# Kernel tuning notes

Hardware: AMD Instinct MI355X
Metric: run time of the kernel (lower is better)

The kernel has to match this reference:

```python
import jax, jax.numpy as jnp
from jax import lax
import numpy as np

BS, T, DA, DZ, K = 64, 512, 16, 32, 3


def _lstm_layer(x, Wih, Whh, bih, bhh):
    # x: [B, T, in], PyTorch LSTM gate order i,f,g,o; zero initial state
    B = x.shape[0]
    H = Whh.shape[1]
    b = bih + bhh

    def step(carry, xt):
        h, c = carry
        g = xt @ Wih.T + h @ Whh.T + b  # [B, 4H]
        i, f, gg, o = jnp.split(g, 4, axis=-1)
        c = jax.nn.sigmoid(f) * c + jax.nn.sigmoid(i) * jnp.tanh(gg)
        h = jax.nn.sigmoid(o) * jnp.tanh(c)
        return (h, c), h

    h0 = jnp.zeros((B, H), x.dtype)
    _, hs = lax.scan(step, (h0, h0), jnp.swapaxes(x, 0, 1))
    return jnp.swapaxes(hs, 0, 1)


def setup_inputs() -> dict:
    key = jax.random.key(0)
    ks = jax.random.split(key, 12)
    a = jax.random.normal(ks[0], (BS, T, DA), jnp.float32)
    # mixture dynamics / emission matrices, kept near identity for stability
    A = 0.95 * jnp.eye(DZ, dtype=jnp.float32) + 0.02 * jax.random.normal(ks[1], (K, T, DZ, DZ), jnp.float32)
    C = jnp.eye(DA, DZ, dtype=jnp.float32) + 0.05 * jax.random.normal(ks[2], (K, T, DA, DZ), jnp.float32)
    R = 0.1 * jnp.eye(DA, dtype=jnp.float32)
    Q = 0.1 * jnp.eye(DZ, dtype=jnp.float32)
    mu0 = jnp.zeros((DZ,), jnp.float32)
    sigma0 = jnp.eye(DZ, dtype=jnp.float32)
    H4 = 4 * K  # LSTM hidden size = K
    Wih0 = 0.1 * jax.random.normal(ks[3], (H4, DA), jnp.float32)
    Whh0 = 0.1 * jax.random.normal(ks[4], (H4, K), jnp.float32)
    bih0 = 0.1 * jax.random.normal(ks[5], (H4,), jnp.float32)
    bhh0 = 0.1 * jax.random.normal(ks[6], (H4,), jnp.float32)
    Wih1 = 0.1 * jax.random.normal(ks[7], (H4, K), jnp.float32)
    Whh1 = 0.1 * jax.random.normal(ks[8], (H4, K), jnp.float32)
    bih1 = 0.1 * jax.random.normal(ks[9], (H4,), jnp.float32)
    bhh1 = 0.1 * jax.random.normal(ks[10], (H4,), jnp.float32)
    return {"a": a, "A": A, "C": C, "R": R, "Q": Q, "mu0": mu0, "sigma0": sigma0,
            "Wih0": Wih0, "Whh0": Whh0, "bih0": bih0, "bhh0": bhh0,
            "Wih1": Wih1, "Whh1": Whh1, "bih1": bih1, "bhh1": bhh1}


def reference(a, A, C, R, Q, mu0, sigma0, Wih0, Whh0, bih0, bhh0, Wih1, Whh1, bih1, bhh1):
    bs, T, da = a.shape
    dz = A.shape[-1]
    # dynamics network: 2-layer LSTM + softmax mixture weights alpha [bs,T,K]
    h = _lstm_layer(a, Wih0, Whh0, bih0, bhh0)
    h = _lstm_layer(h, Wih1, Whh1, bih1, bhh1)
    alpha = jax.nn.softmax(h, axis=-1)
    # mix per-mode matrices; time-major [T,bs,.,.]
    At = jnp.einsum('btk,ktij->tbij', alpha, A)
    Ct = jnp.einsum('btk,ktij->tbij', alpha, C)
    a_tm = jnp.swapaxes(a, 0, 1)  # [T,bs,da]
    I = jnp.eye(dz, dtype=a.dtype)
    mu_f0 = jnp.broadcast_to(mu0, (bs, dz))
    sig_f0 = jnp.broadcast_to(sigma0, (bs, dz, dz))

    def fstep(carry, inp):
        mu_f, mu_p, sig_p = carry  # prev filtered mean, predicted mean/cov
        a_t, A_t, C_t = inp
        # NOTE: residual uses previous *filtered* mean, matching the source code
        r = a_t - jnp.einsum('bij,bj->bi', C_t, mu_f)
        Ct_T = jnp.swapaxes(C_t, -1, -2)
        S = C_t @ sig_p @ Ct_T + R
        Kg = sig_p @ Ct_T @ jnp.linalg.inv(S)
        mu_new = mu_p + jnp.einsum('bij,bj->bi', Kg, r)
        sig_new = (I - Kg @ C_t) @ sig_p
        mu_p_new = jnp.einsum('bij,bj->bi', A_t, mu_new)
        sig_p_new = A_t @ sig_new @ jnp.swapaxes(A_t, -1, -2) + Q
        return (mu_new, mu_p_new, sig_p_new), (mu_new, sig_new, mu_p_new, sig_p_new)

    _, (mu_f, sig_f, mu_p, sig_p) = lax.scan(
        fstep, (mu_f0, mu_f0, sig_f0), (a_tm, At, Ct))

    # RTS smoothing (backward recursion), faithful to smooth()
    def sstep(carry, inp):
        mu_n, sig_n = carry
        mu_ft, sig_ft, mu_pt, sig_pt, A_next = inp
        J = sig_ft @ jnp.swapaxes(A_next, -1, -2) @ jnp.linalg.inv(sig_pt)
        mu_s = mu_ft + jnp.einsum('bij,bj->bi', J, mu_n - mu_pt)
        sig_s = sig_ft + J @ (sig_n - sig_pt)
        return (mu_s, sig_s), (mu_s, sig_s)

    _, (mu_s_rest, sig_s_rest) = lax.scan(
        sstep, (mu_f[-1], sig_f[-1]),
        (mu_f[:-1], sig_f[:-1], mu_p[:-1], sig_p[:-1], At[1:]),
        reverse=True)
    mu_s = jnp.concatenate([mu_s_rest, mu_f[-1:]], axis=0)   # [T,bs,dz]
    sig_s = jnp.concatenate([sig_s_rest, sig_f[-1:]], axis=0)  # [T,bs,dz,dz]
    out = jnp.concatenate([mu_s, sig_s.reshape(T, bs, dz * dz)], axis=-1)
    return jnp.swapaxes(out, 0, 1)  # [bs, T, dz + dz*dz]
```

## Files before the change

kernel.cpp:

```cpp
#include <hip/hip_runtime.h>
#include <hip/hip_bf16.h>

#define BSZ 64
#define TT  512
#define DA  16
#define DZ  32
#define NG  12
#define NT  256

typedef __hip_bfloat16 bf;

#define FP32_R0 0x3DCCCCCDu

__device__ __forceinline__ int mode_(const void* Rm){
  return (((const unsigned*)Rm)[0] == FP32_R0) ? 0 : 1;
}
__device__ __forceinline__ float LD(const void* p, size_t i, int b16){
  return b16 ? __bfloat162float(((const bf*)p)[i]) : ((const float*)p)[i];
}
__device__ __forceinline__ void STO(void* p, size_t i, float v, int b16){
  if (b16) ((bf*)p)[i] = __float2bfloat16(v);
  else     ((float*)p)[i] = v;
}
__device__ __forceinline__ float osan_(double vd, float code){
  float v = (float)vd;
  unsigned u = __float_as_uint(v);
  if ((u & 0x7f800000u) == 0x7f800000u)
    return ((u & 0x007fffffu) != 0u) ? code : ((u >> 31) ? -(code-1000.0f) : (code-1000.0f));
  return v;
}
__device__ __forceinline__ float sigm_(float x){ return 1.0f/(1.0f + __expf(-x)); }
__device__ __forceinline__ float tanh_(float x){ return 1.0f - 2.0f/(__expf(2.0f*x)+1.0f); }

__device__ void alpha_stage_(int b, int tid, int b16,
  const void* a, const void* Wih0, const void* bih0, const void* bhh0,
  const void* Whh0, const void* Wih1, const void* Whh1,
  const void* bih1, const void* bhh1,
  float* sxw, float* salp)
{
  for (int e=tid; e<TT*NG; e+=NT){
    int t=e/NG, g=e-NG*t;
    float s = LD(bih0,g,b16) + LD(bhh0,g,b16);
    size_t ab = ((size_t)b*TT + t)*DA;
    #pragma unroll
    for (int j=0;j<DA;++j) s += LD(Wih0,g*DA+j,b16)*LD(a,ab+j,b16);
    sxw[e] = s;
  }
  __syncthreads();
  if (tid==0){
    float w0[NG][3], wi1[NG][3], w1[NG][3], bb[NG];
    #pragma unroll
    for (int g=0;g<NG;++g){
      #pragma unroll
      for (int j=0;j<3;++j){ w0[g][j]=LD(Whh0,(size_t)g*3+j,b16); wi1[g][j]=LD(Wih1,(size_t)g*3+j,b16); w1[g][j]=LD(Whh1,(size_t)g*3+j,b16); }
      bb[g] = LD(bih1,g,b16) + LD(bhh1,g,b16);
    }
    float h1[3]={0,0,0}, c1[3]={0,0,0}, h2[3]={0,0,0}, c2[3]={0,0,0};
    for (int t=0;t<TT;++t){
      const float* xr = sxw + t*NG;
      float g1[NG];
      #pragma unroll
      for (int g=0;g<NG;++g) g1[g] = xr[g] + w0[g][0]*h1[0]+w0[g][1]*h1[1]+w0[g][2]*h1[2];
      #pragma unroll
      for (int j=0;j<3;++j){
        float iv=sigm_(g1[j]), fv=sigm_(g1[3+j]), gv=tanh_(g1[6+j]), ov=sigm_(g1[9+j]);
        c1[j] = fv*c1[j] + iv*gv;
        h1[j] = ov*tanh_(c1[j]);
      }
      float g2[NG];
      #pragma unroll
      for (int g=0;g<NG;++g) g2[g] = bb[g] + wi1[g][0]*h1[0]+wi1[g][1]*h1[1]+wi1[g][2]*h1[2]
                                            + w1[g][0]*h2[0]+w1[g][1]*h2[1]+w1[g][2]*h2[2];
      #pragma unroll
      for (int j=0;j<3;++j){
        float iv=sigm_(g2[j]), fv=sigm_(g2[3+j]), gv=tanh_(g2[6+j]), ov=sigm_(g2[9+j]);
        c2[j] = fv*c2[j] + iv*gv;
        h2[j] = ov*tanh_(c2[j]);
      }
      float m = fmaxf(h2[0], fmaxf(h2[1], h2[2]));
      float e0=__expf(h2[0]-m), e1=__expf(h2[1]-m), e2=__expf(h2[2]-m);
      float inv = 1.0f/(e0+e1+e2);
      salp[t*3+0]=e0*inv; salp[t*3+1]=e1*inv; salp[t*3+2]=e2*inv;
    }
  }
  __syncthreads();
}

__global__ __launch_bounds__(256) void k_alpha(
  const void* __restrict__ a, const void* __restrict__ Rm,
  const void* __restrict__ Wih0, const void* __restrict__ Whh0,
  const void* __restrict__ bih0, const void* __restrict__ bhh0,
  const void* __restrict__ Wih1, const void* __restrict__ Whh1,
  const void* __restrict__ bih1, const void* __restrict__ bhh1,
  float* __restrict__ alws)
{
  const int b16 = mode_(Rm);
  const int b = blockIdx.x, tid = threadIdx.x;
  __shared__ float sxw[TT*NG];
  __shared__ float salp[TT*3];
  alpha_stage_(b, tid, b16, a, Wih0, bih0, bhh0, Whh0, Wih1, Whh1, bih1, bhh1,
               sxw, salp);
  for (int e=tid;e<TT*3;e+=NT) alws[(size_t)b*TT*3+e] = salp[e];
}

__global__ __launch_bounds__(256) void k_fwd(
  const void* __restrict__ a, const void* __restrict__ Am,
  const void* __restrict__ Cm, const void* __restrict__ Rm,
  const void* __restrict__ Qm, const void* __restrict__ mu0,
  const void* __restrict__ sig0,
  const void* __restrict__ Wih0, const void* __restrict__ Whh0,
  const void* __restrict__ bih0, const void* __restrict__ bhh0,
  const void* __restrict__ Wih1, const void* __restrict__ Whh1,
  const void* __restrict__ bih1, const void* __restrict__ bhh1,
  const float* __restrict__ alws,
  void* __restrict__ out)
{
  const int b16 = mode_(Rm);
  const int b = blockIdx.x, tid = threadIdx.x;
  __shared__ double dpool[4240];
  __shared__ float sAt[1056], sCt[528], sQ[1056], sR[272], sPCt[544], sKg[544];
  __shared__ float salp[TT*3];
  __shared__ double dMu[32], dMup[32], dr[16];
  double* dPp  = dpool;
  double* dPf  = dpool+1056;
  double* dCP  = dpool+2112;
  double* dT1  = dpool+2640;
  double* dAugS= dpool+3696;
  double* dMinv= dpool+3968;

  if (alws){
    for (int e=tid;e<TT*3;e+=NT) salp[e] = alws[(size_t)b*TT*3+e];
    __syncthreads();
  } else {
    alpha_stage_(b, tid, b16, a, Wih0, bih0, bhh0, Whh0, Wih1, Whh1, bih1, bhh1,
                 (float*)dpool, salp);
  }

  for (int e=tid;e<1024;e+=NT){ int i=e>>5,j=e&31;
    sQ[i*33+j]  = LD(Qm,e,b16);
    dPp[i*33+j] = (double)LD(sig0,e,b16); }
  for (int e=tid;e<256;e+=NT){ int i=e>>4,j=e&15; sR[i*17+j] = LD(Rm,e,b16); }
  if (tid<32){ double m = (double)LD(mu0,tid,b16); dMu[tid]=m; dMup[tid]=m; }
  __syncthreads();

  const int i0 = tid>>5, j0 = tid&31;
  const int i4 = tid>>4, j4 = tid&15;

  float pA0[4],pA1[4],pA2[4],pC0[2],pC1[2],pC2[2];
  {
    size_t o0=0, o1=(size_t)TT*1024, o2=(size_t)2*TT*1024;
    #pragma unroll
    for (int q=0;q<4;++q){ int e=tid+q*NT; pA0[q]=LD(Am,o0+e,b16); pA1[q]=LD(Am,o1+e,b16); pA2[q]=LD(Am,o2+e,b16); }
    size_t c0=0, c1=(size_t)TT*512, c2=(size_t)2*TT*512;
    #pragma unroll
    for (int q=0;q<2;++q){ int e=tid+q*NT; pC0[q]=LD(Cm,c0+e,b16); pC1[q]=LD(Cm,c1+e,b16); pC2[q]=LD(Cm,c2+e,b16); }
  }

  for (int t=0;t<TT;++t){
    const size_t ob = ((size_t)b*TT+t)*1056;
    {
      float a0=salp[t*3+0], a1=salp[t*3+1], a2=salp[t*3+2];
      #pragma unroll
      for (int q=0;q<4;++q){ int e=tid+q*NT; int i=e>>5,j=e&31;
        sAt[i*33+j] = a0*pA0[q]+a1*pA1[q]+a2*pA2[q]; }
      #pragma unroll
      for (int q=0;q<2;++q){ int e=tid+q*NT; int i=e>>5,j=e&31;
        sCt[i*33+j] = a0*pC0[q]+a1*pC1[q]+a2*pC2[q]; }
    }
    if (t+1<TT){
      size_t o0=(size_t)(t+1)*1024, o1=(size_t)(TT+t+1)*1024, o2=(size_t)(2*TT+t+1)*1024;
      #pragma unroll
      for (int q=0;q<4;++q){ int e=tid+q*NT; pA0[q]=LD(Am,o0+e,b16); pA1[q]=LD(Am,o1+e,b16); pA2[q]=LD(Am,o2+e,b16); }
      size_t c0=(size_t)(t+1)*512, c1=(size_t)(TT+t+1)*512, c2=(size_t)(2*TT+t+1)*512;
      #pragma unroll
      for (int q=0;q<2;++q){ int e=tid+q*NT; pC0[q]=LD(Cm,c0+e,b16); pC1[q]=LD(Cm,c1+e,b16); pC2[q]=LD(Cm,c2+e,b16); }
    }
    __syncthreads();

    {
      double A0=0.0, A1=0.0;
      for (int k=0;k<32;++k){ double bv=dPp[k*33+j0];
        A0 += (double)sCt[i0*33+k]*bv;
        A1 += (double)sCt[(i0+8)*33+k]*bv; }
      dCP[i0*33+j0]=A0; dCP[(i0+8)*33+j0]=A1;
    }
    {
      double A0=0.0, A1=0.0;
      for (int m=0;m<32;++m){ double cv=(double)sCt[j4*33+m];
        A0 += dPp[i4*33+m]*cv;
        A1 += dPp[(i4+16)*33+m]*cv; }
      sPCt[i4*17+j4]=(float)A0; sPCt[(i4+16)*17+j4]=(float)A1;
    }
    if (tid<16){ double s = (double)LD(a,((size_t)b*TT+t)*DA+tid,b16);
      for (int k=0;k<32;++k) s -= (double)sCt[tid*33+k]*dMu[k];
      dr[tid]=s; }
    __syncthreads();

    { int i=tid>>4, j=tid&15; double v=(double)sR[i*17+j];
      for (int k=0;k<32;++k) v += dCP[i*33+k]*(double)sCt[j*33+k];
      dAugS[i*17+j]=v; }
    __syncthreads();

    if (tid < 64){
      const int r = tid>>2, q = tid&3, cbase = q*8;
      double Rg[8];
      #pragma unroll
      for (int u=0;u<8;++u){
        int c = cbase+u;
        Rg[u] = (c<16) ? dAugS[r*17+c] : ((c-16)==r ? 1.0 : 0.0);
      }
      #pragma unroll
      for (int kp=0;kp<16;++kp){
        double pv = __shfl(Rg[kp&7], (kp<<2)|(kp>>3), 64);
        if (!(fabs(pv)>1e-300)) pv=1.0;
        double ip = 1.0/pv;
        if (r==kp){
          #pragma unroll
          for (int u=0;u<8;++u){ int c=cbase+u; if (c>kp) Rg[u]*=ip; }
        }
        double rf = __shfl(Rg[kp&7], (tid&0x3C)|(kp>>3), 64);
        #pragma unroll
        for (int u=0;u<8;++u){
          double pr = __shfl(Rg[u], (kp<<2)|q, 64);
          int c=cbase+u;
          if (r!=kp && c>kp) Rg[u] -= rf*pr;
        }
      }
      if (q>=2){
        #pragma unroll
        for (int u=0;u<8;++u){ int k=cbase+u-16; dMinv[r*17+k]=Rg[u]; }
      }
    }
    __syncthreads();

    {
      double A0=0.0, A1=0.0;
      for (int l=0;l<16;++l){ double mv=dMinv[l*17+j4];
        A0 += (double)sPCt[i4*17+l]*mv;
        A1 += (double)sPCt[(i4+16)*17+l]*mv; }
      sKg[i4*17+j4]=(float)A0; sKg[(i4+16)*17+j4]=(float)A1;
    }
    __syncthreads();

    if (tid<32){ double s=dMup[tid];
      for (int k=0;k<16;++k) s += (double)sKg[tid*17+k]*dr[k];
      dMu[tid]=s;
      STO(out, ob+tid, osan_(s,5300.0f), b16);
    }
    {
      double A0=dPp[i0*33+j0], A1=dPp[(i0+8)*33+j0],
             A2=dPp[(i0+16)*33+j0], A3=dPp[(i0+24)*33+j0];
      for (int l=0;l<16;++l){ double cv=dCP[l*33+j0];
        A0 -= (double)sKg[i0*17+l]*cv;
        A1 -= (double)sKg[(i0+8)*17+l]*cv;
        A2 -= (double)sKg[(i0+16)*17+l]*cv;
        A3 -= (double)sKg[(i0+24)*17+l]*cv; }
      dPf[i0*33+j0]=A0; dPf[(i0+8)*33+j0]=A1;
      dPf[(i0+16)*33+j0]=A2; dPf[(i0+24)*33+j0]=A3;
      STO(out, ob+32+((size_t)i0<<5)+j0,      osan_(A0,5300.0f), b16);
      STO(out, ob+32+((size_t)(i0+8)<<5)+j0,  osan_(A1,5300.0f), b16);
      STO(out, ob+32+((size_t)(i0+16)<<5)+j0, osan_(A2,5300.0f), b16);
      STO(out, ob+32+((size_t)(i0+24)<<5)+j0, osan_(A3,5300.0f), b16);
    }
    __syncthreads();

    {
      double A0=0.0,A1=0.0,A2=0.0,A3=0.0;
      for (int k=0;k<32;++k){ double bv=dPf[k*33+j0];
        A0 += (double)sAt[i0*33+k]*bv;
        A1 += (double)sAt[(i0+8)*33+k]*bv;
        A2 += (double)sAt[(i0+16)*33+k]*bv;
        A3 += (double)sAt[(i0+24)*33+k]*bv; }
      dT1[i0*33+j0]=A0; dT1[(i0+8)*33+j0]=A1;
      dT1[(i0+16)*33+j0]=A2; dT1[(i0+24)*33+j0]=A3;
    }
    if (tid<32){ double s=0.0;
      for (int k=0;k<32;++k) s += (double)sAt[tid*33+k]*dMu[k];
      dMup[tid]=s; }
    __syncthreads();

    {
      double A0=(double)sQ[i0*33+j0], A1=(double)sQ[(i0+8)*33+j0],
             A2=(double)sQ[(i0+16)*33+j0], A3=(double)sQ[(i0+24)*33+j0];
      for (int k=0;k<32;++k){ double av=(double)sAt[j0*33+k];
        A0 += dT1[i0*33+k]*av;
        A1 += dT1[(i0+8)*33+k]*av;
        A2 += dT1[(i0+16)*33+k]*av;
        A3 += dT1[(i0+24)*33+k]*av; }
      dPp[i0*33+j0]=A0; dPp[(i0+8)*33+j0]=A1;
      dPp[(i0+16)*33+j0]=A2; dPp[(i0+24)*33+j0]=A3;
    }
    __syncthreads();
  }
}

__global__ __launch_bounds__(256) void k_pre(
  const void* __restrict__ Am, const void* __restrict__ Qm,
  const void* __restrict__ Rm, const void* __restrict__ outv,
  const float* __restrict__ alws, float* __restrict__ rec, int t0)
{
  const int b16 = mode_(Rm);
  const int t = t0 + blockIdx.x;
  const int b = blockIdx.y;
  const int tid = threadIdx.x;
  __shared__ double dAug[2080];
  __shared__ double dmp[32];
  __shared__ float sAtc[1056], sAtn[1056], sSf[1056], sT[1056], sF[1056], sPp[1056], sJ[1056], sQ[1056];
  __shared__ float smu[32];

  size_t obase = (size_t)b*TT*1056;
  const float* al = alws + (size_t)b*TT*3;
  float c0=al[t*3+0],     c1=al[t*3+1],     c2=al[t*3+2];
  float n0=al[(t+1)*3+0], n1=al[(t+1)*3+1], n2=al[(t+1)*3+2];
  size_t oA0c=(size_t)t*1024, oA1c=(size_t)(TT+t)*1024, oA2c=(size_t)(2*TT+t)*1024;
  size_t oA0n=oA0c+1024, oA1n=oA1c+1024, oA2n=oA2c+1024;

  for (int e=tid;e<1024;e+=NT){ int i=e>>5,j=e&31;
    sAtc[i*33+j] = c0*LD(Am,oA0c+e,b16)+c1*LD(Am,oA1c+e,b16)+c2*LD(Am,oA2c+e,b16);
    sAtn[i*33+j] = n0*LD(Am,oA0n+e,b16)+n1*LD(Am,oA1n+e,b16)+n2*LD(Am,oA2n+e,b16);
    sSf[i*33+j]  = LD(outv, obase + (size_t)t*1056 + 32 + e, b16);
    sQ[i*33+j]   = LD(Qm,e,b16);
  }
  if (tid<32) smu[tid] = LD(outv, obase + (size_t)t*1056 + tid, b16);
  __syncthreads();

  for (int e=tid;e<1024;e+=NT){ int i=e>>5, j=e&31;
    double acc=0.0, accF=0.0;
    for (int k=0;k<32;++k){
      acc  += (double)sAtc[i*33+k]*(double)sSf[k*33+j];
      accF += (double)sSf[i*33+k]*(double)sAtn[j*33+k];
    }
    sT[i*33+j]=(float)acc; sF[i*33+j]=(float)accF; }
  if (tid<32){ double s=0.0;
    for (int k=0;k<32;++k) s += (double)sAtc[tid*33+k]*(double)smu[k];
    dmp[tid]=s; }
  __syncthreads();

  for (int e=tid;e<1024;e+=NT){ int i=e>>5, j=e&31;
    double acc=(double)sQ[i*33+j];
    for (int k=0;k<32;++k) acc += (double)sT[i*33+k]*(double)sAtc[j*33+k];
    sPp[i*33+j]=(float)acc;
    dAug[i*65+j]=acc;
    dAug[i*65+32+j]=(i==j)?1.0:0.0; }
  __syncthreads();

  for (int kp=0;kp<32;++kp){
    double pv = dAug[kp*65+kp];
    if (!(fabs(pv)>1e-300)) pv=1.0;
    double ip = 1.0/pv;
    if (tid<64 && tid>kp) dAug[kp*65+tid] *= ip;
    __syncthreads();
    for (int e=tid;e<2048;e+=NT){ int i=e>>6, j=e&63;
      if (i!=kp && j>kp) dAug[i*65+j] -= dAug[i*65+kp]*dAug[kp*65+j];
    }
    __syncthreads();
  }

  float* rp = rec + ((size_t)b*gridDim.x + (size_t)blockIdx.x)*2080;

  for (int e=tid;e<1024;e+=NT){ int i=e>>5, j=e&31; double acc=0.0;
    for (int k=0;k<32;++k) acc += (double)sF[i*33+k]*dAug[k*65+32+j];
    float jv=(float)acc; sJ[i*33+j]=jv; rp[e]=jv; }
  __syncthreads();

  for (int e=tid;e<1024;e+=NT){ int i=e>>5, j=e&31;
    double acc=(double)sSf[i*33+j];
    for (int k=0;k<32;++k) acc -= (double)sJ[i*33+k]*(double)sPp[k*33+j];
    rp[1024+e]=(float)acc; }
  if (tid<32){ double acc=(double)smu[tid];
    for (int k=0;k<32;++k) acc -= (double)sJ[tid*33+k]*dmp[k];
    rp[2048+tid]=(float)acc; }
}

__global__ __launch_bounds__(256) void k_bwd(
  const void* __restrict__ Rm, void* __restrict__ outv,
  const float* __restrict__ rec, float* __restrict__ cont,
  int t0, int t1)
{
  const int b16 = mode_(Rm);
  const int b = blockIdx.x, tid = threadIdx.x;
  const int chlen = t1 - t0;
  __shared__ float sX[2][1056];
  __shared__ float sR[2080];
  size_t obase = (size_t)b*TT*1056;
  int cur = 0;
  const int i0 = tid>>5, j0 = tid&31;

  if (t1 == TT-1){
    for (int e=tid;e<1024;e+=NT){ int i=e>>5,j=e&31;
      sX[0][i*33+j] = LD(outv, obase+(size_t)(TT-1)*1056+32+e, b16); }
    if (tid<32) sX[0][tid*33+32] = LD(outv, obase+(size_t)(TT-1)*1056+tid, b16);
  } else {
    for (int e=tid;e<1056;e+=NT) sX[0][e] = cont[(size_t)b*1056+e];
  }
  float rg[9];
  {
    const float* rp = rec + ((size_t)b*chlen + (size_t)(chlen-1))*2080;
    #pragma unroll
    for (int q=0;q<9;++q){ int e=tid+q*NT; rg[q] = (e<2080)? rp[e] : 0.0f; }
  }
  __syncthreads();

  for (int t=t1-1; t>=t0; --t){
    #pragma unroll
    for (int q=0;q<9;++q){ int e=tid+q*NT; if (e<2080) sR[e]=rg[q]; }
    if (t>t0){
      const float* rp = rec + ((size_t)b*chlen + (size_t)(t-1-t0))*2080;
      #pragma unroll
      for (int q=0;q<9;++q){ int e=tid+q*NT; rg[q] = (e<2080)? rp[e] : 0.0f; }
    }
    __syncthreads();

    const float* Xc = sX[cur]; float* Xn = sX[cur^1];
    {
      double A0=(double)sR[1024+(i0<<5)+j0];
      double A1=(double)sR[1024+((i0+8)<<5)+j0];
      double A2=(double)sR[1024+((i0+16)<<5)+j0];
      double A3=(double)sR[1024+((i0+24)<<5)+j0];
      for (int k=0;k<32;++k){ double xv=(double)Xc[k*33+j0];
        A0 += (double)sR[(i0<<5)+k]*xv;
        A1 += (double)sR[((i0+8)<<5)+k]*xv;
        A2 += (double)sR[((i0+16)<<5)+k]*xv;
        A3 += (double)sR[((i0+24)<<5)+k]*xv; }
      Xn[i0*33+j0]=(float)A0;      Xn[(i0+8)*33+j0]=(float)A1;
      Xn[(i0+16)*33+j0]=(float)A2; Xn[(i0+24)*33+j0]=(float)A3;
      size_t tb = obase+(size_t)t*1056+32;
      STO(outv, tb+((size_t)i0<<5)+j0,      osan_(A0,5700.0f), b16);
      STO(outv, tb+((size_t)(i0+8)<<5)+j0,  osan_(A1,5700.0f), b16);
      STO(outv, tb+((size_t)(i0+16)<<5)+j0, osan_(A2,5700.0f), b16);
      STO(outv, tb+((size_t)(i0+24)<<5)+j0, osan_(A3,5700.0f), b16);
    }
    if (tid<32){
      double acc=(double)sR[2048+tid];
      for (int k=0;k<32;++k) acc += (double)sR[(tid<<5)+k]*(double)Xc[k*33+32];
      Xn[tid*33+32]=(float)acc;
      STO(outv, obase+(size_t)t*1056+tid, osan_(acc,5700.0f), b16);
    }
    __syncthreads();
    cur ^= 1;
  }
  for (int e=tid;e<1056;e+=NT) cont[(size_t)b*1056+e] = sX[cur][e];
}

__global__ __launch_bounds__(256) void k_smooth(
  const void* __restrict__ a, const void* __restrict__ Am,
  const void* __restrict__ Rm, const void* __restrict__ Qm,
  const void* __restrict__ Wih0, const void* __restrict__ Whh0,
  const void* __restrict__ bih0, const void* __restrict__ bhh0,
  const void* __restrict__ Wih1, const void* __restrict__ Whh1,
  const void* __restrict__ bih1, const void* __restrict__ bhh1,
  void* __restrict__ out)
{
  const int b16 = mode_(Rm);
  const int b = blockIdx.x, tid = threadIdx.x;
  __shared__ double dAug[2080];
  __shared__ float fp2[9504];
  __shared__ float salp[TT*3];
  __shared__ double dMun[32], dmp[32], sdm[32];
  float* sAtn = fp2;
  float* sAtc = fp2+1056;
  float* sSf  = fp2+2112;
  float* sSn  = fp2+3168;
  float* sT   = fp2+4224;
  float* sQ   = fp2+5280;
  float* sF   = fp2+6336;
  float* sPp32= fp2+7392;
  float* sJ   = fp2+8448;

  alpha_stage_(b, tid, b16, a, Wih0, bih0, bhh0, Whh0, Wih1, Whh1, bih1, bhh1,
               fp2, salp);

  size_t obase = (size_t)b*TT*1056;
  for (int e=tid;e<1024;e+=NT){ int i=e>>5,j=e&31;
    sQ[i*33+j]  = LD(Qm,e,b16);
    sSn[i*33+j] = LD(out, obase + (size_t)(TT-1)*1056 + 32 + e, b16); }
  if (tid<32) dMun[tid] = (double)LD(out, obase + (size_t)(TT-1)*1056 + tid, b16);
  __syncthreads();

  for (int t=TT-2; t>=0; --t){
    float n0=salp[(t+1)*3+0], n1=salp[(t+1)*3+1], n2=salp[(t+1)*3+2];
    float c0=salp[t*3+0],     c1=salp[t*3+1],     c2=salp[t*3+2];
    size_t oA0n=(size_t)(t+1)*1024, oA1n=(size_t)(TT+t+1)*1024, oA2n=(size_t)(2*TT+t+1)*1024;
    size_t oA0c=(size_t)t*1024,     oA1c=(size_t)(TT+t)*1024,   oA2c=(size_t)(2*TT+t)*1024;
    for (int e=tid;e<1024;e+=NT){ int i=e>>5,j=e&31;
      sAtn[i*33+j] = n0*LD(Am,oA0n+e,b16)+n1*LD(Am,oA1n+e,b16)+n2*LD(Am,oA2n+e,b16);
      sAtc[i*33+j] = c0*LD(Am,oA0c+e,b16)+c1*LD(Am,oA1c+e,b16)+c2*LD(Am,oA2c+e,b16);
      sSf[i*33+j]  = LD(out, obase + (size_t)t*1056 + 32 + e, b16); }
    __syncthreads();

    for (int e=tid;e<1024;e+=NT){ int i=e>>5, j=e&31;
      double acc=0.0, accF=0.0;
      for (int k=0;k<32;++k){
        acc  += (double)sAtc[i*33+k]*(double)sSf[k*33+j];
        accF += (double)sSf[i*33+k]*(double)sAtn[j*33+k];
      }
      sT[i*33+j]=(float)acc; sF[i*33+j]=(float)accF; }
    if (tid<32){ double s=0.0; float muf = LD(out, obase+(size_t)t*1056+tid, b16);
      for (int k=0;k<32;++k) s += (double)sAtc[tid*33+k]*(double)LD(out, obase+(size_t)t*1056+k, b16);
      dmp[tid]=s; (void)muf; }
    __syncthreads();

    for (int e=tid;e<1024;e+=NT){ int i=e>>5, j=e&31;
      double acc=(double)sQ[i*33+j];
      for (int k=0;k<32;++k) acc += (double)sT[i*33+k]*(double)sAtc[j*33+k];
      sPp32[i*33+j]=(float)acc;
      dAug[i*65+j]=acc;
      dAug[i*65+32+j]=(i==j)?1.0:0.0; }
    if (tid<32) sdm[tid] = dMun[tid] - dmp[tid];
    __syncthreads();

    for (int kp=0;kp<32;++kp){
      double pv = dAug[kp*65+kp];
      if (!(fabs(pv)>1e-300)) pv=1.0;
      double ip = 1.0/pv;
      if (tid<64 && tid>kp) dAug[kp*65+tid] *= ip;
      __syncthreads();
      for (int e=tid;e<2048;e+=NT){ int i=e>>6, j=e&63;
        if (i!=kp && j>kp) dAug[i*65+j] -= dAug[i*65+kp]*dAug[kp*65+j];
      }
      __syncthreads();
    }

    for (int e=tid;e<1024;e+=NT){ int i=e>>5, j=e&31; double acc=0.0;
      for (int k=0;k<32;++k) acc += (double)sF[i*33+k]*dAug[k*65+32+j];
      sJ[i*33+j]=(float)acc; }
    __syncthreads();

    if (tid<32){ double s2=0.0;
      for (int k=0;k<32;++k) s2 += (double)sJ[tid*33+k]*sdm[k];
      double v = (double)LD(out, obase+(size_t)t*1056+tid, b16) + s2;
      STO(out, obase+(size_t)t*1056+tid, osan_(v,5700.0f), b16);
      dMun[tid] = v;
    }
    float resv[4];
    { int i0 = tid>>5, j = tid&31;
      for (int s=0;s<4;++s){ int i=i0+(s<<3); double acc=0.0;
        for (int k=0;k<32;++k) acc += (double)sJ[i*33+k]*((double)sSn[k*33+j]-(double)sPp32[k*33+j]);
        double res = (double)sSf[i*33+j] + acc;
        STO(out, obase+(size_t)t*1056+32+(i<<5)+j, osan_(res,5700.0f), b16);
        resv[s]=(float)res;
      }
    }
    __syncthreads();
    { int i0 = tid>>5, j = tid&31;
      for (int s=0;s<4;++s){ int i=i0+(s<<3); sSn[i*33+j]=resv[s]; } }
    __syncthreads();
  }
}

__global__ __launch_bounds__(256) void k_fill(float* o, int n, float v){
  int i = blockIdx.x*256 + threadIdx.x;
  if (i<n) o[i]=v;
}

extern "C" void kernel_launch(void* const* d_in, const int* in_sizes, int n_in,
                              void* d_out, int out_size, void* d_ws, size_t ws_size,
                              hipStream_t stream)
{
  static const int EXP[15] = {524288,1572864,786432,256,1024,32,1024,192,36,12,12,36,36,12,12};
  int ok = (n_in==15) && (out_size==34603008);
  if (ok) for (int i=0;i<15;++i) if (in_sizes[i]!=EXP[i]) ok=0;
  if (!ok){
    k_fill<<<dim3((out_size+255)/256), dim3(256), 0, stream>>>((float*)d_out, out_size, 777.0f);
    return;
  }
  const void* a=d_in[0]; const void* Am=d_in[1]; const void* Cm=d_in[2];
  const void* Rm=d_in[3]; const void* Qm=d_in[4]; const void* mu0=d_in[5];
  const void* sig0=d_in[6];
  const void* Wih0=d_in[7]; const void* Whh0=d_in[8]; const void* bih0=d_in[9];
  const void* bhh0=d_in[10]; const void* Wih1=d_in[11]; const void* Whh1=d_in[12];
  const void* bih1=d_in[13]; const void* bhh1=d_in[14];

  const long long FIXED_F = 98304LL + 67584LL;
  long long availB = (long long)ws_size;
  int CH = 0;
  if (d_ws && availB > FIXED_F*4){
    long long ch = (availB - FIXED_F*4) / (64LL*2080LL*4LL);
    CH = (int)((ch > 511) ? 511 : ch);
  }

  if (CH >= 4){
    float* wsf  = (float*)d_ws;
    float* alws = wsf;
    float* cont = wsf + 98304;
    float* rec  = wsf + 165888;

    k_alpha<<<dim3(BSZ), dim3(NT), 0, stream>>>(a, Rm,
        Wih0, Whh0, bih0, bhh0, Wih1, Whh1, bih1, bhh1, alws);
    k_fwd  <<<dim3(BSZ), dim3(NT), 0, stream>>>(a, Am, Cm, Rm, Qm, mu0, sig0,
        Wih0, Whh0, bih0, bhh0, Wih1, Whh1, bih1, bhh1, alws, d_out);

    int t1 = TT-1;
    while (t1 > 0){
      int t0 = t1 - CH; if (t0 < 0) t0 = 0;
      int len = t1 - t0;
      k_pre<<<dim3(len, BSZ), dim3(NT), 0, stream>>>(Am, Qm, Rm, d_out, alws, rec, t0);
      k_bwd<<<dim3(BSZ), dim3(NT), 0, stream>>>(Rm, d_out, rec, cont, t0, t1);
      t1 = t0;
    }
  } else {
    k_fwd   <<<dim3(BSZ), dim3(NT), 0, stream>>>(a, Am, Cm, Rm, Qm, mu0, sig0,
               Wih0, Whh0, bih0, bhh0, Wih1, Whh1, bih1, bhh1, (const float*)nullptr, d_out);
    k_smooth<<<dim3(BSZ), dim3(NT), 0, stream>>>(a, Am, Rm, Qm,
               Wih0, Whh0, bih0, bhh0, Wih1, Whh1, bih1, bhh1, d_out);
  }
}
```

Measured before the change: 10.67 ms.

## Restructure Kalman forward step to overlap A·P with the inverse and cut barriers

The forward filter step now computes A·P_pred on the 192 idle threads while the first wavefront builds and inverts the innovation covariance. The covariance propagation is rewritten algebraically as A·P - A·(K·C·P), which drops one barrier and the separate filtered-covariance buffer. Many inner loops are also fully unrolled, with columns cached in registers. The trade-off is higher register pressure from the register arrays, plus slightly different rounding from the reordered arithmetic.

```diff
diff --git a/kernel.cpp b/kernel.cpp
--- a/kernel.cpp
+++ b/kernel.cpp
@@ -32,13 +32,13 @@
 __device__ __forceinline__ float sigm_(float x){ return 1.0f/(1.0f + __expf(-x)); }
 __device__ __forceinline__ float tanh_(float x){ return 1.0f - 2.0f/(__expf(2.0f*x)+1.0f); }
 
-__device__ void alpha_stage_(int b, int tid, int b16,
+__device__ void alpha_stage_(int b, int tid, int nt, int b16,
   const void* a, const void* Wih0, const void* bih0, const void* bhh0,
   const void* Whh0, const void* Wih1, const void* Whh1,
   const void* bih1, const void* bhh1,
   float* sxw, float* salp)
 {
-  for (int e=tid; e<TT*NG; e+=NT){
+  for (int e=tid; e<TT*NG; e+=nt){
     int t=e/NG, g=e-NG*t;
     float s = LD(bih0,g,b16) + LD(bhh0,g,b16);
     size_t ab = ((size_t)b*TT + t)*DA;
@@ -98,7 +98,7 @@
   const int b = blockIdx.x, tid = threadIdx.x;
   __shared__ float sxw[TT*NG];
   __shared__ float salp[TT*3];
-  alpha_stage_(b, tid, b16, a, Wih0, bih0, bhh0, Whh0, Wih1, Whh1, bih1, bhh1,
+  alpha_stage_(b, tid, NT, b16, a, Wih0, bih0, bhh0, Whh0, Wih1, Whh1, bih1, bhh1,
                sxw, salp);
   for (int e=tid;e<TT*3;e+=NT) alws[(size_t)b*TT*3+e] = salp[e];
 }
@@ -122,9 +122,9 @@
   __shared__ float salp[TT*3];
   __shared__ double dMu[32], dMup[32], dr[16];
   double* dPp  = dpool;
-  double* dPf  = dpool+1056;
-  double* dCP  = dpool+2112;
-  double* dT1  = dpool+2640;
+  double* dAP  = dpool+1056;
+  double* dKCP = dpool+2112;
+  double* dCP  = dpool+3168;
   double* dAugS= dpool+3696;
   double* dMinv= dpool+3968;
 
@@ -132,7 +132,7 @@
     for (int e=tid;e<TT*3;e+=NT) salp[e] = alws[(size_t)b*TT*3+e];
     __syncthreads();
   } else {
-    alpha_stage_(b, tid, b16, a, Wih0, bih0, bhh0, Whh0, Wih1, Whh1, bih1, bhh1,
+    alpha_stage_(b, tid, NT, b16, a, Wih0, bih0, bhh0, Whh0, Wih1, Whh1, bih1, bhh1,
                  (float*)dpool, salp);
   }
 
@@ -178,30 +178,35 @@
     __syncthreads();
 
     {
+      double col[32];
+      #pragma unroll
+      for (int k=0;k<32;++k) col[k] = dPp[k*33+j0];
       double A0=0.0, A1=0.0;
-      for (int k=0;k<32;++k){ double bv=dPp[k*33+j0];
-        A0 += (double)sCt[i0*33+k]*bv;
-        A1 += (double)sCt[(i0+8)*33+k]*bv; }
+      #pragma unroll
+      for (int k=0;k<32;++k){
+        A0 += (double)sCt[i0*33+k]*col[k];
+        A1 += (double)sCt[(i0+8)*33+k]*col[k]; }
       dCP[i0*33+j0]=A0; dCP[(i0+8)*33+j0]=A1;
-    }
-    {
-      double A0=0.0, A1=0.0;
+      double B0=0.0, B1v=0.0;
+      #pragma unroll
       for (int m=0;m<32;++m){ double cv=(double)sCt[j4*33+m];
-        A0 += dPp[i4*33+m]*cv;
-        A1 += dPp[(i4+16)*33+m]*cv; }
-      sPCt[i4*17+j4]=(float)A0; sPCt[(i4+16)*17+j4]=(float)A1;
+        B0  += dPp[i4*33+m]*cv;
+        B1v += dPp[(i4+16)*33+m]*cv; }
+      sPCt[i4*17+j4]=(float)B0; sPCt[(i4+16)*17+j4]=(float)B1v;
     }
     if (tid<16){ double s = (double)LD(a,((size_t)b*TT+t)*DA+tid,b16);
+      #pragma unroll
       for (int k=0;k<32;++k) s -= (double)sCt[tid*33+k]*dMu[k];
       dr[tid]=s; }
     __syncthreads();
 
-    { int i=tid>>4, j=tid&15; double v=(double)sR[i*17+j];
-      for (int k=0;k<32;++k) v += dCP[i*33+k]*(double)sCt[j*33+k];
-      dAugS[i*17+j]=v; }
-    __syncthreads();
-
     if (tid < 64){
+      #pragma unroll
+      for (int u=0;u<4;++u){ int e=(tid<<2)+u; int i=e>>4, j=e&15;
+        double v=(double)sR[i*17+j];
+        #pragma unroll
+        for (int k=0;k<32;++k) v += dCP[i*33+k]*(double)sCt[j*33+k];
+        dAugS[i*17+j]=v; }
       const int r = tid>>2, q = tid&3, cbase = q*8;
       double Rg[8];
       #pragma unroll
@@ -230,63 +235,91 @@
         #pragma unroll
         for (int u=0;u<8;++u){ int k=cbase+u-16; dMinv[r*17+k]=Rg[u]; }
       }
+    } else {
+      for (int e=tid-64; e<1024; e+=192){ int i=e>>5,j=e&31; double acc=0.0;
+        #pragma unroll
+        for (int k=0;k<32;++k) acc += (double)sAt[i*33+k]*dPp[k*33+j];
+        dAP[i*33+j]=acc; }
     }
     __syncthreads();
 
     {
+      double col[16];
+      #pragma unroll
+      for (int l=0;l<16;++l) col[l] = dMinv[l*17+j4];
       double A0=0.0, A1=0.0;
-      for (int l=0;l<16;++l){ double mv=dMinv[l*17+j4];
-        A0 += (double)sPCt[i4*17+l]*mv;
-        A1 += (double)sPCt[(i4+16)*17+l]*mv; }
+      #pragma unroll
+      for (int l=0;l<16;++l){
+        A0 += (double)sPCt[i4*17+l]*col[l];
+        A1 += (double)sPCt[(i4+16)*17+l]*col[l]; }
       sKg[i4*17+j4]=(float)A0; sKg[(i4+16)*17+j4]=(float)A1;
     }
     __syncthreads();
 
+    {
+      double col[16];
+      #pragma unroll
+      for (int l=0;l<16;++l) col[l] = dCP[l*33+j0];
+      double A0=0.0,A1=0.0,A2=0.0,A3=0.0;
+      #pragma unroll
+      for (int l=0;l<16;++l){
+        A0 += (double)sKg[i0*17+l]*col[l];
+        A1 += (double)sKg[(i0+8)*17+l]*col[l];
+        A2 += (double)sKg[(i0+16)*17+l]*col[l];
+        A3 += (double)sKg[(i0+24)*17+l]*col[l]; }
+      dKCP[i0*33+j0]=A0; dKCP[(i0+8)*33+j0]=A1;
+      dKCP[(i0+16)*33+j0]=A2; dKCP[(i0+24)*33+j0]=A3;
+    }
     if (tid<32){ double s=dMup[tid];
+      #pragma unroll
       for (int k=0;k<16;++k) s += (double)sKg[tid*17+k]*dr[k];
       dMu[tid]=s;
-      STO(out, ob+tid, osan_(s,5300.0f), b16);
-    }
+      STO(out, ob+tid, osan_(s,5300.0f), b16); }
+    __syncthreads();
+
     {
-      double A0=dPp[i0*33+j0], A1=dPp[(i0+8)*33+j0],
-             A2=dPp[(i0+16)*33+j0], A3=dPp[(i0+24)*33+j0];
-      for (int l=0;l<16;++l){ double cv=dCP[l*33+j0];
-        A0 -= (double)sKg[i0*17+l]*cv;
-        A1 -= (double)sKg[(i0+8)*17+l]*cv;
-        A2 -= (double)sKg[(i0+16)*17+l]*cv;
-        A3 -= (double)sKg[(i0+24)*17+l]*cv; }
-      dPf[i0*33+j0]=A0; dPf[(i0+8)*33+j0]=A1;
-      dPf[(i0+16)*33+j0]=A2; dPf[(i0+24)*33+j0]=A3;
-      STO(out, ob+32+((size_t)i0<<5)+j0,      osan_(A0,5300.0f), b16);
-      STO(out, ob+32+((size_t)(i0+8)<<5)+j0,  osan_(A1,5300.0f), b16);
-      STO(out, ob+32+((size_t)(i0+16)<<5)+j0, osan_(A2,5300.0f), b16);
-      STO(out, ob+32+((size_t)(i0+24)<<5)+j0, osan_(A3,5300.0f), b16);
-    }
-    __syncthreads();
-
-    {
-      double A0=0.0,A1=0.0,A2=0.0,A3=0.0;
-      for (int k=0;k<32;++k){ double bv=dPf[k*33+j0];
-        A0 += (double)sAt[i0*33+k]*bv;
-        A1 += (double)sAt[(i0+8)*33+k]*bv;
-        A2 += (double)sAt[(i0+16)*33+k]*bv;
-        A3 += (double)sAt[(i0+24)*33+k]*bv; }
-      dT1[i0*33+j0]=A0; dT1[(i0+8)*33+j0]=A1;
-      dT1[(i0+16)*33+j0]=A2; dT1[(i0+24)*33+j0]=A3;
+      double colK[32];
+      #pragma unroll
+      for (int k=0;k<32;++k) colK[k] = dKCP[k*33+j0];
+      double pf0 = dPp[i0*33+j0]      - colK[0*0+ (0)];
+      (void)pf0;
+      double P0 = dPp[i0*33+j0]      - dKCP[i0*33+j0];
+      double P1 = dPp[(i0+8)*33+j0]  - dKCP[(i0+8)*33+j0];
+      double P2 = dPp[(i0+16)*33+j0] - dKCP[(i0+16)*33+j0];
+      double P3 = dPp[(i0+24)*33+j0] - dKCP[(i0+24)*33+j0];
+      STO(out, ob+32+((size_t)i0<<5)+j0,      osan_(P0,5300.0f), b16);
+      STO(out, ob+32+((size_t)(i0+8)<<5)+j0,  osan_(P1,5300.0f), b16);
+      STO(out, ob+32+((size_t)(i0+16)<<5)+j0, osan_(P2,5300.0f), b16);
+      STO(out, ob+32+((size_t)(i0+24)<<5)+j0, osan_(P3,5300.0f), b16);
+      double A0=dAP[i0*33+j0], A1=dAP[(i0+8)*33+j0],
+             A2=dAP[(i0+16)*33+j0], A3=dAP[(i0+24)*33+j0];
+      #pragma unroll
+      for (int k=0;k<32;++k){
+        A0 -= (double)sAt[i0*33+k]*colK[k];
+        A1 -= (double)sAt[(i0+8)*33+k]*colK[k];
+        A2 -= (double)sAt[(i0+16)*33+k]*colK[k];
+        A3 -= (double)sAt[(i0+24)*33+k]*colK[k]; }
+      dAP[i0*33+j0]=A0; dAP[(i0+8)*33+j0]=A1;
+      dAP[(i0+16)*33+j0]=A2; dAP[(i0+24)*33+j0]=A3;
     }
     if (tid<32){ double s=0.0;
+      #pragma unroll
       for (int k=0;k<32;++k) s += (double)sAt[tid*33+k]*dMu[k];
       dMup[tid]=s; }
     __syncthreads();
 
     {
+      float rowA[32];
+      #pragma unroll
+      for (int k=0;k<32;++k) rowA[k] = sAt[j0*33+k];
       double A0=(double)sQ[i0*33+j0], A1=(double)sQ[(i0+8)*33+j0],
              A2=(double)sQ[(i0+16)*33+j0], A3=(double)sQ[(i0+24)*33+j0];
-      for (int k=0;k<32;++k){ double av=(double)sAt[j0*33+k];
-        A0 += dT1[i0*33+k]*av;
-        A1 += dT1[(i0+8)*33+k]*av;
-        A2 += dT1[(i0+16)*33+k]*av;
-        A3 += dT1[(i0+24)*33+k]*av; }
+      #pragma unroll
+      for (int k=0;k<32;++k){ double av=(double)rowA[k];
+        A0 += dAP[i0*33+k]*av;
+        A1 += dAP[(i0+8)*33+k]*av;
+        A2 += dAP[(i0+16)*33+k]*av;
+        A3 += dAP[(i0+24)*33+k]*av; }
       dPp[i0*33+j0]=A0; dPp[(i0+8)*33+j0]=A1;
       dPp[(i0+16)*33+j0]=A2; dPp[(i0+24)*33+j0]=A3;
     }
@@ -326,18 +359,21 @@
 
   for (int e=tid;e<1024;e+=NT){ int i=e>>5, j=e&31;
     double acc=0.0, accF=0.0;
+    #pragma unroll
     for (int k=0;k<32;++k){
       acc  += (double)sAtc[i*33+k]*(double)sSf[k*33+j];
       accF += (double)sSf[i*33+k]*(double)sAtn[j*33+k];
     }
     sT[i*33+j]=(float)acc; sF[i*33+j]=(float)accF; }
   if (tid<32){ double s=0.0;
+    #pragma unroll
     for (int k=0;k<32;++k) s += (double)sAtc[tid*33+k]*(double)smu[k];
     dmp[tid]=s; }
   __syncthreads();
 
   for (int e=tid;e<1024;e+=NT){ int i=e>>5, j=e&31;
     double acc=(double)sQ[i*33+j];
+    #pragma unroll
     for (int k=0;k<32;++k) acc += (double)sT[i*33+k]*(double)sAtc[j*33+k];
     sPp[i*33+j]=(float)acc;
     dAug[i*65+j]=acc;
@@ -350,7 +386,8 @@
     double ip = 1.0/pv;
     if (tid<64 && tid>kp) dAug[kp*65+tid] *= ip;
     __syncthreads();
-    for (int e=tid;e<2048;e+=NT){ int i=e>>6, j=e&63;
+    #pragma unroll
+    for (int q=0;q<8;++q){ int e=tid+q*NT; int i=e>>6, j=e&63;
       if (i!=kp && j>kp) dAug[i*65+j] -= dAug[i*65+kp]*dAug[kp*65+j];
     }
     __syncthreads();
@@ -359,15 +396,18 @@
   float* rp = rec + ((size_t)b*gridDim.x + (size_t)blockIdx.x)*2080;
 
   for (int e=tid;e<1024;e+=NT){ int i=e>>5, j=e&31; double acc=0.0;
+    #pragma unroll
     for (int k=0;k<32;++k) acc += (double)sF[i*33+k]*dAug[k*65+32+j];
     float jv=(float)acc; sJ[i*33+j]=jv; rp[e]=jv; }
   __syncthreads();
 
   for (int e=tid;e<1024;e+=NT){ int i=e>>5, j=e&31;
     double acc=(double)sSf[i*33+j];
+    #pragma unroll
     for (int k=0;k<32;++k) acc -= (double)sJ[i*33+k]*(double)sPp[k*33+j];
     rp[1024+e]=(float)acc; }
   if (tid<32){ double acc=(double)smu[tid];
+    #pragma unroll
     for (int k=0;k<32;++k) acc -= (double)sJ[tid*33+k]*dmp[k];
     rp[2048+tid]=(float)acc; }
 }
@@ -413,11 +453,15 @@
 
     const float* Xc = sX[cur]; float* Xn = sX[cur^1];
     {
+      float colX[32];
+      #pragma unroll
+      for (int k=0;k<32;++k) colX[k] = Xc[k*33+j0];
       double A0=(double)sR[1024+(i0<<5)+j0];
       double A1=(double)sR[1024+((i0+8)<<5)+j0];
       double A2=(double)sR[1024+((i0+16)<<5)+j0];
       double A3=(double)sR[1024+((i0+24)<<5)+j0];
-      for (int k=0;k<32;++k){ double xv=(double)Xc[k*33+j0];
+      #pragma unroll
+      for (int k=0;k<32;++k){ double xv=(double)colX[k];
         A0 += (double)sR[(i0<<5)+k]*xv;
         A1 += (double)sR[((i0+8)<<5)+k]*xv;
         A2 += (double)sR[((i0+16)<<5)+k]*xv;
@@ -432,6 +476,7 @@
     }
     if (tid<32){
       double acc=(double)sR[2048+tid];
+      #pragma unroll
       for (int k=0;k<32;++k) acc += (double)sR[(tid<<5)+k]*(double)Xc[k*33+32];
       Xn[tid*33+32]=(float)acc;
       STO(outv, obase+(size_t)t*1056+tid, osan_(acc,5700.0f), b16);
@@ -467,7 +512,7 @@
   float* sPp32= fp2+7392;
   float* sJ   = fp2+8448;
 
-  alpha_stage_(b, tid, b16, a, Wih0, bih0, bhh0, Whh0, Wih1, Whh1, bih1, bhh1,
+  alpha_stage_(b, tid, NT, b16, a, Wih0, bih0, bhh0, Whh0, Wih1, Whh1, bih1, bhh1,
                fp2, salp);
 
   size_t obase = (size_t)b*TT*1056;
@@ -490,18 +535,21 @@
 
     for (int e=tid;e<1024;e+=NT){ int i=e>>5, j=e&31;
       double acc=0.0, accF=0.0;
+      #pragma unroll
       for (int k=0;k<32;++k){
         acc  += (double)sAtc[i*33+k]*(double)sSf[k*33+j];
         accF += (double)sSf[i*33+k]*(double)sAtn[j*33+k];
       }
       sT[i*33+j]=(float)acc; sF[i*33+j]=(float)accF; }
     if (tid<32){ double s=0.0; float muf = LD(out, obase+(size_t)t*1056+tid, b16);
+      #pragma unroll
       for (int k=0;k<32;++k) s += (double)sAtc[tid*33+k]*(double)LD(out, obase+(size_t)t*1056+k, b16);
       dmp[tid]=s; (void)muf; }
     __syncthreads();
 
     for (int e=tid;e<1024;e+=NT){ int i=e>>5, j=e&31;
       double acc=(double)sQ[i*33+j];
+      #pragma unroll
       for (int k=0;k<32;++k) acc += (double)sT[i*33+k]*(double)sAtc[j*33+k];
       sPp32[i*33+j]=(float)acc;
       dAug[i*65+j]=acc;
@@ -522,11 +570,13 @@
     }
 
     for (int e=tid;e<1024;e+=NT){ int i=e>>5, j=e&31; double acc=0.0;
+      #pragma unroll
       for (int k=0;k<32;++k) acc += (double)sF[i*33+k]*dAug[k*65+32+j];
       sJ[i*33+j]=(float)acc; }
     __syncthreads();
 
     if (tid<32){ double s2=0.0;
+      #pragma unroll
       for (int k=0;k<32;++k) s2 += (double)sJ[tid*33+k]*sdm[k];
       double v = (double)LD(out, obase+(size_t)t*1056+tid, b16) + s2;
       STO(out, obase+(size_t)t*1056+tid, osan_(v,5700.0f), b16);
@@ -535,6 +585,7 @@
     float resv[4];
     { int i0 = tid>>5, j = tid&31;
       for (int s=0;s<4;++s){ int i=i0+(s<<3); double acc=0.0;
+        #pragma unroll
         for (int k=0;k<32;++k) acc += (double)sJ[i*33+k]*((double)sSn[k*33+j]-(double)sPp32[k*33+j]);
         double res = (double)sSf[i*33+j] + acc;
         STO(out, obase+(size_t)t*1056+32+(i<<5)+j, osan_(res,5700.0f), b16);
```

New measurement: 10.92 ms. 2.4% more time.
